# Kernel tuning notes

Hardware: AMD Instinct MI355X
Metric: run time of the kernel (lower is better)

Reference implementation:

```python
import jax, jax.numpy as jnp
import numpy as np

MINIMUM_VALUE = -1e9  # C.MINIMUM_VALUE: large negative fill for masked positions


def setup_inputs() -> dict:
    key = jax.random.key(0)
    kq, kv, km, kw = jax.random.split(key, 4)
    B, N, H = 8, 2048, 1024
    query = jax.random.normal(kq, (B, N, H), dtype=jnp.float32)
    value = jax.random.normal(kv, (B, N, H), dtype=jnp.float32)
    mask = jax.random.randint(km, (B, N, N), 0, 2, dtype=jnp.int32)
    W = jax.random.normal(kw, (H, H), dtype=jnp.float32)
    return {"query": query, "value": value, "mask": mask, "W": W}


def reference(query, value, mask, W):
    # intermediate = query @ W           : B x M x H
    # e = relu(intermediate @ value^T)   : B x M x N
    e = jax.nn.relu(jnp.einsum("bmh,hk,bnk->bmn", query, W, value))
    attn_logits = jnp.where(mask > 0, e, MINIMUM_VALUE)
    attn = jax.nn.softmax(attn_logits, axis=-1)
    output = jnp.einsum("bmn,bnh->bmh", attn, value)
    return (output, attn)
```

## Files before the change

### kernel.cpp

```cpp
#include <hip/hip_runtime.h>


typedef _Float16 half8 __attribute__((ext_vector_type(8)));
typedef float f32x4 __attribute__((ext_vector_type(4)));
typedef unsigned short u16;
typedef unsigned int u32;

#define BATCH 8
#define SEQ   2048
#define HID   1024
#define MINV  (-1e9f)

#define AS1 __attribute__((address_space(1)))
#define AS3 __attribute__((address_space(3)))

__device__ __forceinline__ u16 h2u(_Float16 h) { return __builtin_bit_cast(u16, h); }

__device__ __forceinline__ u32 packhl(float x) {
    _Float16 h = (_Float16)x;
    _Float16 l = (_Float16)(x - (float)h);
    return (u32)h2u(h) | ((u32)h2u(l) << 16);
}

__device__ __forceinline__ void gload16(const char* g, AS3 char* l) {
    __builtin_amdgcn_global_load_lds((const AS1 void*)g, (AS3 void*)l, 16, 0, 0);
}

__global__ __launch_bounds__(256) void prep_v(const float* __restrict__ V,
                                              u16* __restrict__ Vp,
                                              u16* __restrict__ Vt)
{
    __shared__ __align__(16) u16 lt[64 * 72];
    const int b = blockIdx.z, n0 = blockIdx.y * 64, h0 = blockIdx.x * 64;
    const int t = threadIdx.x;
    const int r = t >> 4, c4 = (t & 15) * 4;
#pragma unroll
    for (int it = 0; it < 4; ++it) {
        const int rr = r + it * 16;
        const float4 x = *(const float4*)(V + ((size_t)b * SEQ + n0 + rr) * HID + h0 + c4);
        const float xs[4] = {x.x, x.y, x.z, x.w};
        u32 p[4];
#pragma unroll
        for (int e = 0; e < 4; ++e) {
            p[e] = packhl(xs[e]);
            lt[(c4 + e) * 72 + rr] = (u16)p[e];
        }
        const int g = (h0 + c4) >> 5, j = c4 & 31;
        u16* base = Vp + (((size_t)b * SEQ + n0 + rr) * 32 + g) * 64;
        *(uint2*)(base + j) = make_uint2((p[0] & 0xffffu) | (p[1] << 16),
                                         (p[2] & 0xffffu) | (p[3] << 16));
        *(uint2*)(base + 32 + j) = make_uint2((p[0] >> 16) | (p[1] & 0xffff0000u),
                                              (p[2] >> 16) | (p[3] & 0xffff0000u));
    }
    __syncthreads();
    const int hr = t >> 2, cc = (t & 3) * 2;
    uint4 v0 = *(const uint4*)&lt[hr * 72 + cc * 8];
    uint4 v1 = *(const uint4*)&lt[hr * 72 + cc * 8 + 8];
    u16* dst = Vt + ((size_t)b * HID + h0 + hr) * SEQ + n0 + cc * 8;
    *(uint4*)dst = v0;
    *(uint4*)(dst + 8) = v1;
}

__global__ __launch_bounds__(256) void prep_w(const float* __restrict__ W,
                                              u16* __restrict__ Wtp)
{
    __shared__ __align__(16) u32 lt[64 * 68];
    const int n0 = blockIdx.x * 64, k0 = blockIdx.y * 64;
    const int t = threadIdx.x;
    const int r = t >> 4, c4 = (t & 15) * 4;
#pragma unroll
    for (int it = 0; it < 4; ++it) {
        const int rr = r + it * 16;
        const float4 x = *(const float4*)(W + (size_t)(k0 + rr) * HID + n0 + c4);
        const float xs[4] = {x.x, x.y, x.z, x.w};
#pragma unroll
        for (int e = 0; e < 4; ++e) lt[(c4 + e) * 68 + rr] = packhl(xs[e]);
    }
    __syncthreads();
    const int n = t >> 2;
#pragma unroll
    for (int s = 0; s < 4; ++s) {
        const int ci = (t & 3) + s * 4;
        uint4 v = *(const uint4*)&lt[n * 68 + ci * 4];
        const int k = k0 + ci * 4;
        u16* base = Wtp + (((size_t)n0 + n) * 32 + (k >> 5)) * 64;
        const int j = k & 31;
        *(uint2*)(base + j) = make_uint2((v.x & 0xffffu) | (v.y << 16),
                                         (v.z & 0xffffu) | (v.w << 16));
        *(uint2*)(base + 32 + j) = make_uint2((v.x >> 16) | (v.y & 0xffff0000u),
                                              (v.z >> 16) | (v.w & 0xffff0000u));
    }
}

__global__ __launch_bounds__(256) void prep_q(const float* __restrict__ Q,
                                              u16* __restrict__ Qp)
{
    const size_t row = blockIdx.x;
    const int t = threadIdx.x;
    const float4 x = ((const float4*)(Q + row * HID))[t];
    const u32 p0 = packhl(x.x), p1 = packhl(x.y), p2 = packhl(x.z), p3 = packhl(x.w);
    const int k = t * 4;
    u16* base = Qp + (row * 32 + (k >> 5)) * 64;
    const int j = k & 31;
    *(uint2*)(base + j) = make_uint2((p0 & 0xffffu) | (p1 << 16),
                                     (p2 & 0xffffu) | (p3 << 16));
    *(uint2*)(base + 32 + j) = make_uint2((p0 >> 16) | (p1 & 0xffff0000u),
                                          (p2 >> 16) | (p3 & 0xffff0000u));
}

template <bool SPLIT>
__device__ __forceinline__ void cluster4x2(f32x4 (&acc)[8][4], int ib, int jb,
                                           const half8 (&ah)[4], const half8 (&al)[4],
                                           half8 bh0, half8 bl0, half8 bh1, half8 bl1)
{
#pragma unroll
    for (int f = 0; f < 4; ++f) {
#pragma unroll
        for (int jj = 0; jj < 2; ++jj) {
            const half8 bh = jj ? bh1 : bh0;
            const half8 bl = jj ? bl1 : bl0;
            f32x4 c = acc[ib + f][jb + jj];
            if constexpr (SPLIT) {
                c = __builtin_amdgcn_mfma_f32_16x16x32_f16(al[f], bh, c, 0, 0, 0);
                c = __builtin_amdgcn_mfma_f32_16x16x32_f16(ah[f], bl, c, 0, 0, 0);
                c = __builtin_amdgcn_mfma_f32_16x16x32_f16(ah[f], bh, c, 0, 0, 0);
            } else {
                c = __builtin_amdgcn_mfma_f32_16x16x32_f16(ah[f], bh, c, 0, 0, 0);
                c = __builtin_amdgcn_mfma_f32_16x16x32_f16(al[f], bl, c, 0, 0, 0);
            }
            acc[ib + f][jb + jj] = c;
        }
    }
}

template <int MODE>
__global__ __launch_bounds__(512, 2) void gemm_mfma(
    const char* __restrict__ Abase, const char* __restrict__ Bbase,
    void* __restrict__ Cbase, const int* __restrict__ Mbase,
    int ldc, long sAb, long sBb, long sC, long sM)
{
    constexpr bool SPLIT = (MODE != 3);
    extern __shared__ __align__(16) char smem[];

    const int nx = gridDim.x, ny = gridDim.y;
    const int nxy = nx * ny;
    int wg = blockIdx.x + nx * (blockIdx.y + ny * blockIdx.z);
    const int cpx = (nxy * gridDim.z) >> 3;
    wg = (wg & 7) * cpx + (wg >> 3);
    const int bz = wg / nxy;
    const int rem = wg - bz * nxy;
    const int m0 = (rem / nx) * 256, n0 = (rem % nx) * 256;

    const int tid = threadIdx.x;
    const int w = tid >> 6, l = tid & 63;
    const int wm = w >> 2, wn = w & 3;
    const int lm = l & 15, q = l >> 4;

    const char* Ab = Abase + (long)bz * sAb;
    const char* Bb = Bbase + (long)bz * sBb;

    size_t aoffs[4], boffs[4];
    int dsto[4];
#pragma unroll
    for (int it = 0; it < 4; ++it) {
        const int off = it * 8192 + tid * 16;
        dsto[it] = off;
        const int row = off >> 7;
        const int swi = (off & 127) ^ ((row & 7) << 4);
        aoffs[it] = (size_t)(m0 + row) * 4096 + swi;
        boffs[it] = (size_t)(n0 + row) * 4096 + swi;
    }
    const int wofs = (q * 16) ^ ((lm & 7) << 4);

    f32x4 acc[8][4];
#pragma unroll
    for (int i = 0; i < 8; ++i)
#pragma unroll
        for (int j = 0; j < 4; ++j) acc[i][j] = (f32x4){0.f, 0.f, 0.f, 0.f};

    AS3 char* lds = (AS3 char*)smem;

#pragma unroll
    for (int it = 0; it < 4; ++it) gload16(Ab + aoffs[it], lds + dsto[it]);
#pragma unroll
    for (int it = 0; it < 4; ++it) gload16(Bb + boffs[it], lds + 32768 + dsto[it]);
    asm volatile("s_waitcnt vmcnt(0)" ::: "memory");
    __builtin_amdgcn_s_barrier();

    half8 ah[4], al[4];
    half8 b0h, b0l, b1h, b1l, b2h, b2l, b3h, b3l;

    for (int ks = 0; ks < 32; ++ks) {
        const int cur = ks & 1;
        const char* At = smem + cur * 65536;
        const char* Bt = At + 32768;
        AS3 char* ldsA = lds + (cur ^ 1) * 65536;
        AS3 char* ldsB = ldsA + 32768;
        const size_t kb = (size_t)(ks + 1) * 128;
        const bool more = (ks < 31);

#pragma unroll
        for (int i = 0; i < 4; ++i) {
            const char* rp = At + ((i >> 1) * 64 + wm * 32 + (i & 1) * 16 + lm) * 128;
            ah[i] = *(const half8*)(rp + wofs);
            al[i] = *(const half8*)(rp + (wofs ^ 64));
        }
        {
            const char* cp0 = Bt + (wn * 32 + lm) * 128;
            b0h = *(const half8*)(cp0 + wofs);
            b0l = *(const half8*)(cp0 + (wofs ^ 64));
            const char* cp1 = Bt + (wn * 32 + 16 + lm) * 128;
            b1h = *(const half8*)(cp1 + wofs);
            b1l = *(const half8*)(cp1 + (wofs ^ 64));
        }
        if (more) {
            gload16(Ab + aoffs[0] + kb, ldsA + dsto[0]);
            gload16(Ab + aoffs[1] + kb, ldsA + dsto[1]);
            gload16(Bb + boffs[0] + kb, ldsB + dsto[0]);
            gload16(Bb + boffs[1] + kb, ldsB + dsto[1]);
            asm volatile("s_waitcnt vmcnt(6)" ::: "memory");
        } else {
            asm volatile("s_waitcnt vmcnt(2)" ::: "memory");
        }
        __builtin_amdgcn_s_barrier();
        asm volatile("s_waitcnt lgkmcnt(0)" ::: "memory");
        __builtin_amdgcn_sched_barrier(0);
        __builtin_amdgcn_s_setprio(1);
        cluster4x2<SPLIT>(acc, 0, 0, ah, al, b0h, b0l, b1h, b1l);
        __builtin_amdgcn_s_setprio(0);
        __builtin_amdgcn_s_barrier();

        {
            const char* cp2 = Bt + (128 + wn * 32 + lm) * 128;
            b2h = *(const half8*)(cp2 + wofs);
            b2l = *(const half8*)(cp2 + (wofs ^ 64));
            const char* cp3 = Bt + (128 + wn * 32 + 16 + lm) * 128;
            b3h = *(const half8*)(cp3 + wofs);
            b3l = *(const half8*)(cp3 + (wofs ^ 64));
        }
        if (more) {
            gload16(Bb + boffs[2] + kb, ldsB + dsto[2]);
            gload16(Bb + boffs[3] + kb, ldsB + dsto[3]);
            asm volatile("s_waitcnt vmcnt(6)" ::: "memory");
        } else {
            asm volatile("s_waitcnt vmcnt(0)" ::: "memory");
        }
        __builtin_amdgcn_s_barrier();
        asm volatile("s_waitcnt lgkmcnt(0)" ::: "memory");
        __builtin_amdgcn_sched_barrier(0);
        __builtin_amdgcn_s_setprio(1);
        cluster4x2<SPLIT>(acc, 0, 2, ah, al, b2h, b2l, b3h, b3l);
        __builtin_amdgcn_s_setprio(0);
        __builtin_amdgcn_s_barrier();

#pragma unroll
        for (int i = 0; i < 4; ++i) {
            const char* rp = At + (128 + (i >> 1) * 64 + wm * 32 + (i & 1) * 16 + lm) * 128;
            ah[i] = *(const half8*)(rp + wofs);
            al[i] = *(const half8*)(rp + (wofs ^ 64));
        }
        if (more) {
            gload16(Ab + aoffs[2] + kb, ldsA + dsto[2]);
            gload16(Ab + aoffs[3] + kb, ldsA + dsto[3]);
        }
        __builtin_amdgcn_s_barrier();
        asm volatile("s_waitcnt lgkmcnt(0)" ::: "memory");
        __builtin_amdgcn_sched_barrier(0);
        __builtin_amdgcn_s_setprio(1);
        cluster4x2<SPLIT>(acc, 4, 2, ah, al, b2h, b2l, b3h, b3l);
        __builtin_amdgcn_s_setprio(0);
        __builtin_amdgcn_s_barrier();

        if (more) asm volatile("s_waitcnt vmcnt(4)" ::: "memory");
        __builtin_amdgcn_s_barrier();
        __builtin_amdgcn_s_setprio(1);
        cluster4x2<SPLIT>(acc, 4, 0, ah, al, b0h, b0l, b1h, b1l);
        __builtin_amdgcn_s_setprio(0);
        __builtin_amdgcn_s_barrier();
    }

#pragma unroll
    for (int i = 0; i < 8; ++i) {
        const int arow = (i >> 1) * 64 + wm * 32 + (i & 1) * 16 + q * 4;
#pragma unroll
        for (int r = 0; r < 4; ++r) {
            const int grow = m0 + arow + r;
#pragma unroll
            for (int j = 0; j < 4; ++j) {
                const int gcol = n0 + (j >> 1) * 128 + wn * 32 + (j & 1) * 16 + lm;
                const float v = acc[i][j][r];
                if constexpr (MODE == 1) {
                    const u32 p = packhl(v);
                    u16* base = (u16*)Cbase + ((size_t)grow * (ldc >> 5) + (gcol >> 5)) * 64;
                    base[gcol & 31] = (u16)p;
                    base[32 + (gcol & 31)] = (u16)(p >> 16);
                } else if constexpr (MODE == 2) {
                    const int mv = Mbase[(long)bz * sM + (long)grow * ldc + gcol];
                    ((float*)Cbase)[(long)bz * sC + (long)grow * ldc + gcol] =
                        (mv > 0) ? fmaxf(v, 0.f) : MINV;
                } else {
                    ((float*)Cbase)[(long)bz * sC + (long)grow * ldc + gcol] = v;
                }
            }
        }
    }
}

__global__ __launch_bounds__(256) void softmax2048(float* __restrict__ attn,
                                                   u16* __restrict__ attnH)
{
    const long row = blockIdx.x;
    float* p = attn + row * 2048;
    const int tid = threadIdx.x;

    float4 v0 = ((const float4*)p)[tid];
    float4 v1 = ((const float4*)p)[tid + 256];

    float mx = fmaxf(fmaxf(fmaxf(v0.x, v0.y), fmaxf(v0.z, v0.w)),
                     fmaxf(fmaxf(v1.x, v1.y), fmaxf(v1.z, v1.w)));
#pragma unroll
    for (int o = 32; o >= 1; o >>= 1)
        mx = fmaxf(mx, __shfl_xor(mx, o, 64));

    __shared__ float redm[4];
    __shared__ float reds[4];
    const int wid = tid >> 6, lane = tid & 63;
    if (lane == 0) redm[wid] = mx;
    __syncthreads();
    mx = fmaxf(fmaxf(redm[0], redm[1]), fmaxf(redm[2], redm[3]));

    float e[8];
    e[0] = __expf(v0.x - mx); e[1] = __expf(v0.y - mx);
    e[2] = __expf(v0.z - mx); e[3] = __expf(v0.w - mx);
    e[4] = __expf(v1.x - mx); e[5] = __expf(v1.y - mx);
    e[6] = __expf(v1.z - mx); e[7] = __expf(v1.w - mx);

    float s = ((e[0] + e[1]) + (e[2] + e[3])) + ((e[4] + e[5]) + (e[6] + e[7]));
#pragma unroll
    for (int o = 32; o >= 1; o >>= 1)
        s += __shfl_xor(s, o, 64);
    if (lane == 0) reds[wid] = s;
    __syncthreads();
    s = (reds[0] + reds[1]) + (reds[2] + reds[3]);

    const float inv = 1.0f / s;
    float o0 = e[0] * inv, o1 = e[1] * inv, o2 = e[2] * inv, o3 = e[3] * inv;
    float o4 = e[4] * inv, o5 = e[5] * inv, o6 = e[6] * inv, o7 = e[7] * inv;
    ((float4*)p)[tid]       = make_float4(o0, o1, o2, o3);
    ((float4*)p)[tid + 256] = make_float4(o4, o5, o6, o7);

    u16* ph = attnH + row * 2048;
    ((uint2*)ph)[tid] =
        make_uint2((u32)h2u((_Float16)o0) | ((u32)h2u((_Float16)o1) << 16),
                   (u32)h2u((_Float16)o2) | ((u32)h2u((_Float16)o3) << 16));
    ((uint2*)ph)[tid + 256] =
        make_uint2((u32)h2u((_Float16)o4) | ((u32)h2u((_Float16)o5) << 16),
                   (u32)h2u((_Float16)o6) | ((u32)h2u((_Float16)o7) << 16));
}

extern "C" void kernel_launch(void* const* d_in, const int* in_sizes, int n_in,
                              void* d_out, int out_size, void* d_ws, size_t ws_size,
                              hipStream_t stream)
{
    (void)in_sizes; (void)n_in; (void)out_size; (void)ws_size;

    const float* query = (const float*)d_in[0];
    const float* value = (const float*)d_in[1];
    const int*   mask  = (const int*)d_in[2];
    const float* W     = (const float*)d_in[3];

    float* out  = (float*)d_out;
    float* attn = out + (size_t)BATCH * SEQ * HID;

    u16* Vp  = (u16*)d_ws;
    u16* Vt  = (u16*)((char*)d_ws + ((size_t)64 << 20));
    u16* Wtp = (u16*)((char*)d_ws + ((size_t)96 << 20));

    u16* interP = (u16*)d_out;
    u16* Qp     = (u16*)attn;
    u16* attnH  = Vp;

    static int attr_done = 0;
    if (!attr_done) {
        hipFuncSetAttribute((const void*)gemm_mfma<1>,
                            hipFuncAttributeMaxDynamicSharedMemorySize, 131072);
        hipFuncSetAttribute((const void*)gemm_mfma<2>,
                            hipFuncAttributeMaxDynamicSharedMemorySize, 131072);
        hipFuncSetAttribute((const void*)gemm_mfma<3>,
                            hipFuncAttributeMaxDynamicSharedMemorySize, 131072);
        attr_done = 1;
    }

    prep_v<<<dim3(HID / 64, SEQ / 64, BATCH), 256, 0, stream>>>(value, Vp, Vt);
    prep_w<<<dim3(HID / 64, HID / 64, 1), 256, 0, stream>>>(W, Wtp);
    prep_q<<<dim3(BATCH * SEQ), 256, 0, stream>>>(query, Qp);

    gemm_mfma<1><<<dim3(HID / 256, (BATCH * SEQ) / 256, 1), 512, 131072, stream>>>(
        (const char*)Qp, (const char*)Wtp, interP, nullptr,
        HID, 0, 0, 0, 0);

    gemm_mfma<2><<<dim3(SEQ / 256, SEQ / 256, BATCH), 512, 131072, stream>>>(
        (const char*)interP, (const char*)Vp, attn, mask,
        SEQ, (long)SEQ * 4096, (long)SEQ * 4096, (long)SEQ * SEQ, (long)SEQ * SEQ);

    softmax2048<<<dim3(BATCH * SEQ), 256, 0, stream>>>(attn, attnH);

    gemm_mfma<3><<<dim3(HID / 256, SEQ / 256, BATCH), 512, 131072, stream>>>(
        (const char*)attnH, (const char*)Vt, out, nullptr,
        HID, (long)SEQ * 4096, (long)HID * 4096, (long)SEQ * HID, 0);
}
```

Before: 717.2 us.

## Restructure GEMM k-loop: issue all prefetches up front, one barrier per step

Rewrites the main k-loop schedule. All B fragment LDS reads for the step are loaded together, all eight global-to-LDS prefetches are issued at once, and the interleaved per-quarter barriers and vmcnt waits are replaced by a single vmcnt(0) plus barrier at the end of each iteration. Global offsets also become 32-bit instead of size_t to cut address arithmetic and register use. The aim is to remove barrier and synchronization overhead between MFMA clusters, at the cost of coarser overlap and a full drain of global loads every step.

```diff
diff --git a/kernel.cpp b/kernel.cpp
--- a/kernel.cpp
+++ b/kernel.cpp
@@ -159,7 +159,7 @@
     const char* Ab = Abase + (long)bz * sAb;
     const char* Bb = Bbase + (long)bz * sBb;
 
-    size_t aoffs[4], boffs[4];
+    u32 aoffs[4], boffs[4];
     int dsto[4];
 #pragma unroll
     for (int it = 0; it < 4; ++it) {
@@ -167,8 +167,8 @@
         dsto[it] = off;
         const int row = off >> 7;
         const int swi = (off & 127) ^ ((row & 7) << 4);
-        aoffs[it] = (size_t)(m0 + row) * 4096 + swi;
-        boffs[it] = (size_t)(n0 + row) * 4096 + swi;
+        aoffs[it] = (u32)(m0 + row) * 4096u + (u32)swi;
+        boffs[it] = (u32)(n0 + row) * 4096u + (u32)swi;
     }
     const int wofs = (q * 16) ^ ((lm & 7) << 4);
 
@@ -196,7 +196,7 @@
         const char* Bt = At + 32768;
         AS3 char* ldsA = lds + (cur ^ 1) * 65536;
         AS3 char* ldsB = ldsA + 32768;
-        const size_t kb = (size_t)(ks + 1) * 128;
+        const u32 kb = (u32)(ks + 1) * 128u;
         const bool more = (ks < 31);
 
 #pragma unroll
@@ -212,25 +212,6 @@
             const char* cp1 = Bt + (wn * 32 + 16 + lm) * 128;
             b1h = *(const half8*)(cp1 + wofs);
             b1l = *(const half8*)(cp1 + (wofs ^ 64));
-        }
-        if (more) {
-            gload16(Ab + aoffs[0] + kb, ldsA + dsto[0]);
-            gload16(Ab + aoffs[1] + kb, ldsA + dsto[1]);
-            gload16(Bb + boffs[0] + kb, ldsB + dsto[0]);
-            gload16(Bb + boffs[1] + kb, ldsB + dsto[1]);
-            asm volatile("s_waitcnt vmcnt(6)" ::: "memory");
-        } else {
-            asm volatile("s_waitcnt vmcnt(2)" ::: "memory");
-        }
-        __builtin_amdgcn_s_barrier();
-        asm volatile("s_waitcnt lgkmcnt(0)" ::: "memory");
-        __builtin_amdgcn_sched_barrier(0);
-        __builtin_amdgcn_s_setprio(1);
-        cluster4x2<SPLIT>(acc, 0, 0, ah, al, b0h, b0l, b1h, b1l);
-        __builtin_amdgcn_s_setprio(0);
-        __builtin_amdgcn_s_barrier();
-
-        {
             const char* cp2 = Bt + (128 + wn * 32 + lm) * 128;
             b2h = *(const half8*)(cp2 + wofs);
             b2l = *(const half8*)(cp2 + (wofs ^ 64));
@@ -239,19 +220,23 @@
             b3l = *(const half8*)(cp3 + (wofs ^ 64));
         }
         if (more) {
-            gload16(Bb + boffs[2] + kb, ldsB + dsto[2]);
-            gload16(Bb + boffs[3] + kb, ldsB + dsto[3]);
-            asm volatile("s_waitcnt vmcnt(6)" ::: "memory");
-        } else {
-            asm volatile("s_waitcnt vmcnt(0)" ::: "memory");
-        }
-        __builtin_amdgcn_s_barrier();
+#pragma unroll
+            for (int it = 0; it < 4; ++it) gload16(Ab + (aoffs[it] + kb), ldsA + dsto[it]);
+#pragma unroll
+            for (int it = 0; it < 4; ++it) gload16(Bb + (boffs[it] + kb), ldsB + dsto[it]);
+        }
+
+        asm volatile("s_waitcnt lgkmcnt(4)" ::: "memory");
+        __builtin_amdgcn_sched_barrier(0);
+        __builtin_amdgcn_s_setprio(1);
+        cluster4x2<SPLIT>(acc, 0, 0, ah, al, b0h, b0l, b1h, b1l);
+        __builtin_amdgcn_s_setprio(0);
+
         asm volatile("s_waitcnt lgkmcnt(0)" ::: "memory");
         __builtin_amdgcn_sched_barrier(0);
         __builtin_amdgcn_s_setprio(1);
         cluster4x2<SPLIT>(acc, 0, 2, ah, al, b2h, b2l, b3h, b3l);
         __builtin_amdgcn_s_setprio(0);
-        __builtin_amdgcn_s_barrier();
 
 #pragma unroll
         for (int i = 0; i < 4; ++i) {
@@ -259,23 +244,15 @@
             ah[i] = *(const half8*)(rp + wofs);
             al[i] = *(const half8*)(rp + (wofs ^ 64));
         }
-        if (more) {
-            gload16(Ab + aoffs[2] + kb, ldsA + dsto[2]);
-            gload16(Ab + aoffs[3] + kb, ldsA + dsto[3]);
-        }
-        __builtin_amdgcn_s_barrier();
         asm volatile("s_waitcnt lgkmcnt(0)" ::: "memory");
         __builtin_amdgcn_sched_barrier(0);
         __builtin_amdgcn_s_setprio(1);
         cluster4x2<SPLIT>(acc, 4, 2, ah, al, b2h, b2l, b3h, b3l);
-        __builtin_amdgcn_s_setprio(0);
-        __builtin_amdgcn_s_barrier();
-
-        if (more) asm volatile("s_waitcnt vmcnt(4)" ::: "memory");
-        __builtin_amdgcn_s_barrier();
-        __builtin_amdgcn_s_setprio(1);
         cluster4x2<SPLIT>(acc, 4, 0, ah, al, b0h, b0l, b1h, b1l);
         __builtin_amdgcn_s_setprio(0);
+        __builtin_amdgcn_sched_barrier(0);
+
+        asm volatile("s_waitcnt vmcnt(0)" ::: "memory");
         __builtin_amdgcn_s_barrier();
     }
 
```

Measured after the change: 728.8 us. About the same (+1.6%).
